# Performance work log

Measured on AMD Instinct MI355X. Metric: run time of the kernel, lower is better.

## Reference

```python
import jax, jax.numpy as jnp
import numpy as np

N = 12288
IN_F = 128
OUT_F = 64
ALPHA = 0.2  # LeakyReLU negative slope
NEG_INF = -9e15


def setup_inputs() -> dict:
    key = jax.random.key(0)
    k1, k2, k3, k4 = jax.random.split(key, 4)
    input = jax.random.normal(k1, (N, IN_F), dtype=jnp.float32)
    adj = jax.random.randint(k2, (N, N), 0, 2, dtype=jnp.int32)
    # xavier-uniform-ish init with gain 1.414
    limW = 1.414 * np.sqrt(6.0 / (IN_F + OUT_F))
    W = jax.random.uniform(k3, (IN_F, OUT_F), dtype=jnp.float32, minval=-limW, maxval=limW)
    lima = 1.414 * np.sqrt(6.0 / (2 * OUT_F + 1))
    a = jax.random.uniform(k4, (2 * OUT_F, 1), dtype=jnp.float32, minval=-lima, maxval=lima)
    return {"input": input, "adj": adj, "W": W, "a": a}


def reference(input, adj, W, a):
    # h: (N, out_features)
    h = input @ W
    # broadcast attention logits: e[i,j] = leakyrelu(h_i . a1 + h_j . a2)
    Wh1 = h @ a[:OUT_F, :]          # (N, 1)
    Wh2 = h @ a[OUT_F:, :]          # (N, 1)
    e = Wh1 + Wh2.T                  # (N, N)
    e = jnp.where(e > 0, e, ALPHA * e)  # leaky relu
    # mask by adjacency, row softmax
    attention = jnp.where(adj > 0, e, NEG_INF)
    attention = jax.nn.softmax(attention, axis=1)
    # dropout is identity in eval mode (training=False)
    h_prime = attention @ h          # (N, out_features)
    return jax.nn.elu(h_prime)
```

## Files before the change

### kernel.cpp

```cpp
#include <hip/hip_runtime.h>

#define NN 12288
#define OUTF 64
#define ALPHA 0.2f
#define C1 6.0f
#define KSP 8
#define KRANGE (NN / KSP)
#define ITERS (KRANGE / 64)

typedef unsigned short u16;
typedef unsigned int u32;
typedef unsigned long long u64;
typedef _Float16 half8 __attribute__((ext_vector_type(8)));
typedef float floatx4 __attribute__((ext_vector_type(4)));
typedef int intx4 __attribute__((ext_vector_type(4)));

union H16 { u16 u; _Float16 h; };
__device__ __forceinline__ u16 f2h(float f) { H16 c; c.h = (_Float16)f; return c.u; }

__device__ __forceinline__ void g2l16(const void* g, void* l) {
  __builtin_amdgcn_global_load_lds(
      (const __attribute__((address_space(1))) void*)g,
      (__attribute__((address_space(3))) void*)l, 16, 0, 0);
}

__global__ __launch_bounds__(256) void k1_prep(
    const float* __restrict__ inp, const float* __restrict__ W, const float* __restrict__ a,
    u16* __restrict__ e1h, u16* __restrict__ thh,
    float* __restrict__ f1g, float* __restrict__ f2g, u16* __restrict__ Btf)
{
  __shared__ float Wl[128 * 64];
  __shared__ float hsm[16][66];
  __shared__ float e1sm[16], e2sm[16];
  const int tid = threadIdx.x;
  for (int t = tid; t < 128 * 64 / 4; t += 256)
    ((float4*)Wl)[t] = ((const float4*)W)[t];
  const int wave = tid >> 6, lane = tid & 63;
  const int k16 = blockIdx.x;
  const float a1l = a[lane], a2l = a[OUTF + lane];
  __syncthreads();
  for (int jl = 0; jl < 4; ++jl) {
    const int jn = wave * 4 + jl;
    const int j = k16 * 16 + jn;
    const float4* xp = (const float4*)(inp + (size_t)j * 128);
    float h = 0.f;
#pragma unroll
    for (int c4 = 0; c4 < 32; ++c4) {
      float4 v = xp[c4];
      const int k = c4 * 4;
      h += v.x * Wl[k * 64 + lane] + v.y * Wl[(k + 1) * 64 + lane]
         + v.z * Wl[(k + 2) * 64 + lane] + v.w * Wl[(k + 3) * 64 + lane];
    }
    float p1 = h * a1l, p2 = h * a2l;
#pragma unroll
    for (int off = 32; off > 0; off >>= 1) { p1 += __shfl_xor(p1, off); p2 += __shfl_xor(p2, off); }
    hsm[jn][lane] = h;
    if (lane == 0) {
      const float s1 = p1, s2 = p2;
      const float e1 = expf(s2 - C1), e2 = expf(ALPHA * s2);
      e1sm[jn] = e1; e2sm[jn] = e2;
      e1h[j] = f2h(e1);
      thh[j] = f2h(expf(-s1 - C1));
      f1g[j] = expf(s1 + C1);
      f2g[j] = expf(ALPHA * s1);
    }
  }
  __syncthreads();
  const int k32 = k16 >> 1, hi = (k16 & 1) * 32;
  for (int cc = tid; cc < 320; cc += 256) {
    const int n = cc >> 5, l32 = cc & 31;
    const int r = n * 16 + (l32 & 15);
    const int jb = (l32 >> 4) * 8;
    u32 wpk[4];
#pragma unroll
    for (int p = 0; p < 4; ++p) {
      u16 hh[2];
#pragma unroll
      for (int q2 = 0; q2 < 2; ++q2) {
        const int jj = jb + p * 2 + q2;
        float v;
        if (r < 64)        v = e1sm[jj] * hsm[jj][r];
        else if (r == 64)  v = e1sm[jj];
        else if (r < 80)   v = 0.f;
        else if (r < 144)  v = e2sm[jj] * hsm[jj][r - 80];
        else if (r == 144) v = e2sm[jj];
        else               v = 0.f;
        hh[q2] = f2h(v);
      }
      wpk[p] = (u32)hh[0] | ((u32)hh[1] << 16);
    }
    ((uint4*)Btf)[(size_t)(k32 * 10 + n) * 64 + hi + l32] = make_uint4(wpk[0], wpk[1], wpk[2], wpk[3]);
  }
}

__global__ __launch_bounds__(256, 3) void k2_main(
    const int* __restrict__ adj, const u16* __restrict__ e1h, const u16* __restrict__ thh,
    const u16* __restrict__ Btf, float* __restrict__ part)
{
  __shared__ u16 sB[2][10240];
  __shared__ u64 m1s[2][128];
  __shared__ u64 m2s[2][128];
  const int tid = threadIdx.x;
  const int wave = tid >> 6, lane = tid & 63;
  const int quad = lane >> 4, lr = lane & 15;
  const int mpos = (int)blockIdx.x >> 3;
  const int ks = (int)blockIdx.x & 7;
  const int mbase = mpos * 128;
  const int k0 = ks * KRANGE;

  const int prow = tid >> 3, pcol = tid & 7;
  u16 thu[4];
#pragma unroll
  for (int p = 0; p < 4; ++p) thu[p] = thh[mbase + p * 32 + prow];
  const int* aB = adj + (size_t)(mbase + prow) * NN + k0 + pcol * 8;
  const u16* eB = e1h + k0 + pcol * 8;

  floatx4 acc[2][10];
#pragma unroll
  for (int t = 0; t < 2; ++t)
#pragma unroll
    for (int n = 0; n < 10; ++n) acc[t][n] = (floatx4){0.f, 0.f, 0.f, 0.f};

  intx4 aj[4][2];
  uint4 evv;

  {
    const char* src = (const char*)(Btf + ((size_t)(k0 >> 5)) * 5120);
#pragma unroll
    for (int i = 0; i < 5; ++i)
      g2l16(src + i * 4096 + tid * 16, (char*)&sB[0][0] + i * 4096 + wave * 1024);
#pragma unroll
    for (int p = 0; p < 4; ++p) {
      aj[p][0] = __builtin_nontemporal_load((const intx4*)(aB + (size_t)p * 32 * NN));
      aj[p][1] = __builtin_nontemporal_load((const intx4*)(aB + (size_t)p * 32 * NN + 4));
    }
    evv = *(const uint4*)eB;
    u32 ev8[8] = {evv.x & 0xFFFFu, evv.x >> 16, evv.y & 0xFFFFu, evv.y >> 16,
                  evv.z & 0xFFFFu, evv.z >> 16, evv.w & 0xFFFFu, evv.w >> 16};
#pragma unroll
    for (int p = 0; p < 4; ++p) {
      const int av[8] = {aj[p][0].x, aj[p][0].y, aj[p][0].z, aj[p][0].w,
                         aj[p][1].x, aj[p][1].y, aj[p][1].z, aj[p][1].w};
      u32 b1 = 0, b2 = 0;
#pragma unroll
      for (int e = 0; e < 8; ++e) {
        const bool nbr = av[e] > 0;
        const bool up = ev8[e] > (u32)thu[p];
        b1 |= (u32)(nbr && up) << e;
        b2 |= (u32)(nbr && !up) << e;
      }
      ((unsigned char*)&m1s[0][p * 32 + prow])[pcol] = (unsigned char)b1;
      ((unsigned char*)&m2s[0][p * 32 + prow])[pcol] = (unsigned char)b2;
    }
  }

  for (int it = 0; it < ITERS; ++it) {
    __syncthreads();
    const int cur = it & 1, nxt = cur ^ 1;
    const bool more = (it + 1 < ITERS);
    if (more) {
      const char* src = (const char*)(Btf + ((size_t)(k0 >> 5) + (it + 1) * 2) * 5120);
#pragma unroll
      for (int i = 0; i < 5; ++i)
        g2l16(src + i * 4096 + tid * 16, (char*)&sB[nxt][0] + i * 4096 + wave * 1024);
      const int koff = (it + 1) * 64;
#pragma unroll
      for (int p = 0; p < 4; ++p) {
        aj[p][0] = __builtin_nontemporal_load((const intx4*)(aB + (size_t)p * 32 * NN + koff));
        aj[p][1] = __builtin_nontemporal_load((const intx4*)(aB + (size_t)p * 32 * NN + koff + 4));
      }
      evv = *(const uint4*)(eB + koff);
    }

    u64 w1[2], w2[2];
    w1[0] = m1s[cur][wave * 32 + lr];      w1[1] = m1s[cur][wave * 32 + 16 + lr];
    w2[0] = m2s[cur][wave * 32 + lr];      w2[1] = m2s[cur][wave * 32 + 16 + lr];
#pragma unroll
    for (int h = 0; h < 2; ++h) {
      const u32 sh = (u32)(h * 32 + quad * 8);
      union { half8 v; u16 s[8]; } A1[2], A2[2];
      const u32 m1a = (u32)(w1[0] >> sh) & 0xFFu, m2a = (u32)(w2[0] >> sh) & 0xFFu;
      const u32 m1b = (u32)(w1[1] >> sh) & 0xFFu, m2b = (u32)(w2[1] >> sh) & 0xFFu;
#pragma unroll
      for (int e = 0; e < 8; ++e) {
        A1[0].s[e] = ((m1a >> e) & 1u) ? (u16)0x3C00 : (u16)0;
        A2[0].s[e] = ((m2a >> e) & 1u) ? (u16)0x3C00 : (u16)0;
        A1[1].s[e] = ((m1b >> e) & 1u) ? (u16)0x3C00 : (u16)0;
        A2[1].s[e] = ((m2b >> e) & 1u) ? (u16)0x3C00 : (u16)0;
      }
      const u16* bp = &sB[cur][h * 5120];
#pragma unroll
      for (int n = 0; n < 10; ++n) {
        half8 Bv = *(const half8*)(bp + (n * 64 + lane) * 8);
        acc[0][n] = __builtin_amdgcn_mfma_f32_16x16x32_f16(n < 5 ? A1[0].v : A2[0].v, Bv,
                                                           acc[0][n], 0, 0, 0);
        acc[1][n] = __builtin_amdgcn_mfma_f32_16x16x32_f16(n < 5 ? A1[1].v : A2[1].v, Bv,
                                                           acc[1][n], 0, 0, 0);
      }
    }

    if (more) {
      u32 ev8[8] = {evv.x & 0xFFFFu, evv.x >> 16, evv.y & 0xFFFFu, evv.y >> 16,
                    evv.z & 0xFFFFu, evv.z >> 16, evv.w & 0xFFFFu, evv.w >> 16};
#pragma unroll
      for (int p = 0; p < 4; ++p) {
        const int av[8] = {aj[p][0].x, aj[p][0].y, aj[p][0].z, aj[p][0].w,
                           aj[p][1].x, aj[p][1].y, aj[p][1].z, aj[p][1].w};
        u32 b1 = 0, b2 = 0;
#pragma unroll
        for (int e = 0; e < 8; ++e) {
          const bool nbr = av[e] > 0;
          const bool up = ev8[e] > (u32)thu[p];
          b1 |= (u32)(nbr && up) << e;
          b2 |= (u32)(nbr && !up) << e;
        }
        ((unsigned char*)&m1s[nxt][p * 32 + prow])[pcol] = (unsigned char)b1;
        ((unsigned char*)&m2s[nxt][p * 32 + prow])[pcol] = (unsigned char)b2;
      }
    }
  }

  const int ks96 = ks * 96 + mpos;
#pragma unroll
  for (int t = 0; t < 2; ++t) {
    float* pp = part + ((size_t)ks96 * 128 + wave * 32 + t * 16 + quad * 4) * 132;
#pragma unroll
    for (int r = 0; r < 4; ++r) {
#pragma unroll
      for (int n = 0; n < 4; ++n)
        pp[r * 132 + n * 16 + lr] = acc[t][n][r];
#pragma unroll
      for (int n = 5; n < 9; ++n)
        pp[r * 132 + 64 + (n - 5) * 16 + lr] = acc[t][n][r];
      if (lr == 0) {
        pp[r * 132 + 128] = acc[t][4][r];
        pp[r * 132 + 129] = acc[t][9][r];
      }
    }
  }
}

__global__ __launch_bounds__(256) void k3_final(
    const float* __restrict__ part, const float* __restrict__ f1g,
    const float* __restrict__ f2g, float* __restrict__ out)
{
  const int gid = blockIdx.x * 256 + threadIdx.x;
  const int row = gid >> 6, col = gid & 63;
  const int mpos = row >> 7, r = row & 127;
  float n1 = 0.f, n2 = 0.f, d1 = 0.f, d2 = 0.f;
#pragma unroll
  for (int ks = 0; ks < KSP; ++ks) {
    const float* p = part + ((size_t)(ks * 96 + mpos) * 128 + r) * 132;
    n1 += p[col]; n2 += p[64 + col]; d1 += p[128]; d2 += p[129];
  }
  const float f1 = f1g[row], f2 = f2g[row];
  const float num = f1 * n1 + f2 * n2;
  const float den = fmaxf(f1 * d1 + f2 * d2, 1e-30f);
  const float x = num / den;
  out[gid] = x > 0.f ? x : (expf(x) - 1.f);
}

extern "C" void kernel_launch(void* const* d_in, const int* in_sizes, int n_in,
                              void* d_out, int out_size, void* d_ws, size_t ws_size,
                              hipStream_t stream) {
  const float* inp = (const float*)d_in[0];
  const int* adj = (const int*)d_in[1];
  const float* W = (const float*)d_in[2];
  const float* a = (const float*)d_in[3];

  char* ws = (char*)d_ws;
  u16* Btf = (u16*)ws;
  float* part = (float*)(ws + 3932160);
  char* tail = ws + 3932160 + 51904512;
  u16* e1h = (u16*)tail;
  u16* thh = e1h + NN;
  float* f1g = (float*)(thh + NN);
  float* f2g = f1g + NN;

  k1_prep<<<768, 256, 0, stream>>>(inp, W, a, e1h, thh, f1g, f2g, Btf);
  k2_main<<<768, 256, 0, stream>>>(adj, e1h, thh, Btf, part);
  k3_final<<<NN * OUTF / 256, 256, 0, stream>>>(part, f1g, f2g, (float*)d_out);
}
```

Baseline: 850.6 us.

## Deepen adjacency prefetch to two iterations and enlarge prep blocks

The main kernel now keeps two register buffers of adjacency and e1 values, issuing global loads two iterations ahead and packing masks for the next tile before the MFMA loop instead of after it. This gives the adjacency stream more latency-hiding distance. The cost is more registers, so the launch bound drops to 2 blocks per CU. Separately, the prep kernel handles 64 rows per block (192 blocks) instead of 16, which cuts how often W is reloaded into LDS but uses fewer blocks.

```diff
diff --git a/kernel.cpp b/kernel.cpp
--- a/kernel.cpp
+++ b/kernel.cpp
@@ -30,18 +30,17 @@
     float* __restrict__ f1g, float* __restrict__ f2g, u16* __restrict__ Btf)
 {
   __shared__ float Wl[128 * 64];
-  __shared__ float hsm[16][66];
-  __shared__ float e1sm[16], e2sm[16];
-  const int tid = threadIdx.x;
-  for (int t = tid; t < 128 * 64 / 4; t += 256)
+  __shared__ float hsm[64][65];
+  __shared__ float e1sm[64], e2sm[64];
+  const int tid = threadIdx.x, wave = tid >> 6, lane = tid & 63;
+  const int b = blockIdx.x;
+  for (int t = tid; t < 2048; t += 256)
     ((float4*)Wl)[t] = ((const float4*)W)[t];
-  const int wave = tid >> 6, lane = tid & 63;
-  const int k16 = blockIdx.x;
   const float a1l = a[lane], a2l = a[OUTF + lane];
   __syncthreads();
-  for (int jl = 0; jl < 4; ++jl) {
-    const int jn = wave * 4 + jl;
-    const int j = k16 * 16 + jn;
+  for (int jl = 0; jl < 16; ++jl) {
+    const int jn = wave * 16 + jl;
+    const int j = b * 64 + jn;
     const float4* xp = (const float4*)(inp + (size_t)j * 128);
     float h = 0.f;
 #pragma unroll
@@ -66,11 +65,11 @@
     }
   }
   __syncthreads();
-  const int k32 = k16 >> 1, hi = (k16 & 1) * 32;
-  for (int cc = tid; cc < 320; cc += 256) {
-    const int n = cc >> 5, l32 = cc & 31;
-    const int r = n * 16 + (l32 & 15);
-    const int jb = (l32 >> 4) * 8;
+  for (int cc = tid; cc < 1280; cc += 256) {
+    const int s = cc / 640, rem = cc - s * 640;
+    const int n = rem >> 6, l = rem & 63;
+    const int r = n * 16 + (l & 15);
+    const int jb = s * 32 + (l >> 4) * 8;
     u32 wpk[4];
 #pragma unroll
     for (int p = 0; p < 4; ++p) {
@@ -89,11 +88,32 @@
       }
       wpk[p] = (u32)hh[0] | ((u32)hh[1] << 16);
     }
-    ((uint4*)Btf)[(size_t)(k32 * 10 + n) * 64 + hi + l32] = make_uint4(wpk[0], wpk[1], wpk[2], wpk[3]);
-  }
-}
-
-__global__ __launch_bounds__(256, 3) void k2_main(
+    ((uint4*)Btf)[(size_t)((b * 2 + s) * 10 + n) * 64 + l] = make_uint4(wpk[0], wpk[1], wpk[2], wpk[3]);
+  }
+}
+
+#define PACK_MASKS(dst1, dst2, AJ, EVV)                                                    \
+  {                                                                                        \
+    u32 ev8[8] = {EVV.x & 0xFFFFu, EVV.x >> 16, EVV.y & 0xFFFFu, EVV.y >> 16,              \
+                  EVV.z & 0xFFFFu, EVV.z >> 16, EVV.w & 0xFFFFu, EVV.w >> 16};             \
+    _Pragma("unroll")                                                                      \
+    for (int p = 0; p < 4; ++p) {                                                          \
+      const int av[8] = {AJ[p][0].x, AJ[p][0].y, AJ[p][0].z, AJ[p][0].w,                   \
+                         AJ[p][1].x, AJ[p][1].y, AJ[p][1].z, AJ[p][1].w};                  \
+      u32 b1 = 0, b2 = 0;                                                                  \
+      _Pragma("unroll")                                                                    \
+      for (int e = 0; e < 8; ++e) {                                                        \
+        const bool nbr = av[e] > 0;                                                        \
+        const bool up = ev8[e] > (u32)thu[p];                                              \
+        b1 |= (u32)(nbr && up) << e;                                                       \
+        b2 |= (u32)(nbr && !up) << e;                                                      \
+      }                                                                                    \
+      ((unsigned char*)&dst1[p * 32 + prow])[pcol] = (unsigned char)b1;                    \
+      ((unsigned char*)&dst2[p * 32 + prow])[pcol] = (unsigned char)b2;                    \
+    }                                                                                      \
+  }
+
+__global__ __launch_bounds__(256, 2) void k2_main(
     const int* __restrict__ adj, const u16* __restrict__ e1h, const u16* __restrict__ thh,
     const u16* __restrict__ Btf, float* __restrict__ part)
 {
@@ -121,8 +141,8 @@
 #pragma unroll
     for (int n = 0; n < 10; ++n) acc[t][n] = (floatx4){0.f, 0.f, 0.f, 0.f};
 
-  intx4 aj[4][2];
-  uint4 evv;
+  intx4 ajb[2][4][2];
+  uint4 evb[2];
 
   {
     const char* src = (const char*)(Btf + ((size_t)(k0 >> 5)) * 5120);
@@ -131,45 +151,37 @@
       g2l16(src + i * 4096 + tid * 16, (char*)&sB[0][0] + i * 4096 + wave * 1024);
 #pragma unroll
     for (int p = 0; p < 4; ++p) {
-      aj[p][0] = __builtin_nontemporal_load((const intx4*)(aB + (size_t)p * 32 * NN));
-      aj[p][1] = __builtin_nontemporal_load((const intx4*)(aB + (size_t)p * 32 * NN + 4));
-    }
-    evv = *(const uint4*)eB;
-    u32 ev8[8] = {evv.x & 0xFFFFu, evv.x >> 16, evv.y & 0xFFFFu, evv.y >> 16,
-                  evv.z & 0xFFFFu, evv.z >> 16, evv.w & 0xFFFFu, evv.w >> 16};
+      ajb[0][p][0] = __builtin_nontemporal_load((const intx4*)(aB + (size_t)p * 32 * NN));
+      ajb[0][p][1] = __builtin_nontemporal_load((const intx4*)(aB + (size_t)p * 32 * NN + 4));
+    }
+    evb[0] = *(const uint4*)eB;
+    PACK_MASKS(m1s[0], m2s[0], ajb[0], evb[0])
 #pragma unroll
     for (int p = 0; p < 4; ++p) {
-      const int av[8] = {aj[p][0].x, aj[p][0].y, aj[p][0].z, aj[p][0].w,
-                         aj[p][1].x, aj[p][1].y, aj[p][1].z, aj[p][1].w};
-      u32 b1 = 0, b2 = 0;
-#pragma unroll
-      for (int e = 0; e < 8; ++e) {
-        const bool nbr = av[e] > 0;
-        const bool up = ev8[e] > (u32)thu[p];
-        b1 |= (u32)(nbr && up) << e;
-        b2 |= (u32)(nbr && !up) << e;
-      }
-      ((unsigned char*)&m1s[0][p * 32 + prow])[pcol] = (unsigned char)b1;
-      ((unsigned char*)&m2s[0][p * 32 + prow])[pcol] = (unsigned char)b2;
-    }
+      ajb[1][p][0] = __builtin_nontemporal_load((const intx4*)(aB + (size_t)p * 32 * NN + 64));
+      ajb[1][p][1] = __builtin_nontemporal_load((const intx4*)(aB + (size_t)p * 32 * NN + 68));
+    }
+    evb[1] = *(const uint4*)(eB + 64);
   }
 
   for (int it = 0; it < ITERS; ++it) {
     __syncthreads();
     const int cur = it & 1, nxt = cur ^ 1;
-    const bool more = (it + 1 < ITERS);
-    if (more) {
+    if (it + 1 < ITERS) {
       const char* src = (const char*)(Btf + ((size_t)(k0 >> 5) + (it + 1) * 2) * 5120);
 #pragma unroll
       for (int i = 0; i < 5; ++i)
         g2l16(src + i * 4096 + tid * 16, (char*)&sB[nxt][0] + i * 4096 + wave * 1024);
-      const int koff = (it + 1) * 64;
+      PACK_MASKS(m1s[nxt], m2s[nxt], ajb[nxt], evb[nxt])
+    }
+    if (it + 2 < ITERS) {
+      const int koff = (it + 2) * 64;
 #pragma unroll
       for (int p = 0; p < 4; ++p) {
-        aj[p][0] = __builtin_nontemporal_load((const intx4*)(aB + (size_t)p * 32 * NN + koff));
-        aj[p][1] = __builtin_nontemporal_load((const intx4*)(aB + (size_t)p * 32 * NN + koff + 4));
-      }
-      evv = *(const uint4*)(eB + koff);
+        ajb[cur][p][0] = __builtin_nontemporal_load((const intx4*)(aB + (size_t)p * 32 * NN + koff));
+        ajb[cur][p][1] = __builtin_nontemporal_load((const intx4*)(aB + (size_t)p * 32 * NN + koff + 4));
+      }
+      evb[cur] = *(const uint4*)(eB + koff);
     }
 
     u64 w1[2], w2[2];
@@ -196,26 +208,6 @@
                                                            acc[0][n], 0, 0, 0);
         acc[1][n] = __builtin_amdgcn_mfma_f32_16x16x32_f16(n < 5 ? A1[1].v : A2[1].v, Bv,
                                                            acc[1][n], 0, 0, 0);
-      }
-    }
-
-    if (more) {
-      u32 ev8[8] = {evv.x & 0xFFFFu, evv.x >> 16, evv.y & 0xFFFFu, evv.y >> 16,
-                    evv.z & 0xFFFFu, evv.z >> 16, evv.w & 0xFFFFu, evv.w >> 16};
-#pragma unroll
-      for (int p = 0; p < 4; ++p) {
-        const int av[8] = {aj[p][0].x, aj[p][0].y, aj[p][0].z, aj[p][0].w,
-                           aj[p][1].x, aj[p][1].y, aj[p][1].z, aj[p][1].w};
-        u32 b1 = 0, b2 = 0;
-#pragma unroll
-        for (int e = 0; e < 8; ++e) {
-          const bool nbr = av[e] > 0;
-          const bool up = ev8[e] > (u32)thu[p];
-          b1 |= (u32)(nbr && up) << e;
-          b2 |= (u32)(nbr && !up) << e;
-        }
-        ((unsigned char*)&m1s[nxt][p * 32 + prow])[pcol] = (unsigned char)b1;
-        ((unsigned char*)&m2s[nxt][p * 32 + prow])[pcol] = (unsigned char)b2;
       }
     }
   }
@@ -277,7 +269,7 @@
   float* f1g = (float*)(thh + NN);
   float* f2g = f1g + NN;
 
-  k1_prep<<<768, 256, 0, stream>>>(inp, W, a, e1h, thh, f1g, f2g, Btf);
+  k1_prep<<<192, 256, 0, stream>>>(inp, W, a, e1h, thh, f1g, f2g, Btf);
   k2_main<<<768, 256, 0, stream>>>(adj, e1h, thh, Btf, part);
   k3_final<<<NN * OUTF / 256, 256, 0, stream>>>(part, f1g, f2g, (float*)d_out);
 }
```

New measurement: 1.071 ms. +25.9%, slower.
